# Performance work log

Hardware: AMD Instinct MI355X
Metric: run time of the kernel (lower is better)

Reference implementation:

```python
import jax, jax.numpy as jnp
import numpy as np

DIM = 384
HEADS = 6
NEG = -1e9  # masked-score fill; equivalent to gathering only kept K/V rows


def setup_inputs() -> dict:
    key = jax.random.key(0)
    ks = jax.random.split(key, 9)
    B, N, C = 1, 4098, DIM
    x = jax.random.normal(ks[0], (B, N, C), dtype=jnp.float32)
    pos = jax.random.normal(ks[1], (B, N + 1, C), dtype=jnp.float32)
    # float mask in [0,1); >=0.5 means 'foreground / keep as key', <0.5 pooled into back token
    mask = jax.random.uniform(ks[2], (B, 1, N - 2), dtype=jnp.float32)
    mask_block = jnp.ones((N + 1,), dtype=jnp.float32)  # positions 0, N-1, N always kept
    Wq = jax.random.normal(ks[3], (C, C), dtype=jnp.float32) * 0.02
    Wk = jax.random.normal(ks[4], (C, C), dtype=jnp.float32) * 0.02
    Wv = jax.random.normal(ks[5], (C, C), dtype=jnp.float32) * 0.02
    Wp = jax.random.normal(ks[6], (C, C), dtype=jnp.float32) * 0.02
    bp = jnp.zeros((C,), dtype=jnp.float32)
    return {"x": x, "pos": pos, "mask": mask, "mask_block": mask_block,
            "Wq": Wq, "Wk": Wk, "Wv": Wv, "Wp": Wp, "bp": bp}


def reference(x, pos, mask, mask_block, Wq, Wk, Wv, Wp, bp):
    B, N, C = x.shape
    H = HEADS
    D = C // H
    scale = D ** -0.5
    eps = 1e-10

    # back token: average of background (mask < 0.5) interior tokens
    reverse = jnp.where(mask < 0.5, 1.0, 0.0)                      # (B,1,N-2)
    pooled = jnp.einsum('bon,bnc->boc', reverse, x[:, 1:N - 1])    # (B,1,C)
    back_tokens = pooled / (reverse.sum(axis=2, keepdims=True) + eps)

    kv_x = jnp.concatenate([x, back_tokens], axis=1)               # (B,N+1,C)
    q_x = x + pos[:, :N]
    k_x = kv_x + pos

    q = (q_x @ Wq.T).reshape(B, N, H, D).transpose(0, 2, 1, 3)       # (B,H,N,D)
    k = (k_x @ Wk.T).reshape(B, N + 1, H, D).transpose(0, 2, 1, 3)   # (B,H,N+1,D)
    v = (kv_x @ Wv.T).reshape(B, N + 1, H, D).transpose(0, 2, 1, 3)  # (B,H,N+1,D)

    # key-selection mask: original gathers rows with mask_block >= 0.5;
    # masked softmax over all N+1 keys is mathematically identical.
    mb = mask_block.at[1:N - 1].set(mask[0, 0])
    keep = mb >= 0.5                                               # (N+1,)

    scores = jnp.einsum('bhqd,bhkd->bhqk', q, k) * scale
    scores = jnp.where(keep[None, None, None, :], scores, NEG)
    attn = jax.nn.softmax(scores, axis=-1)
    out = jnp.einsum('bhqk,bhkd->bhqd', attn, v)
    out = out.transpose(0, 2, 1, 3).reshape(B, N, C)
    return out @ Wp.T + bp
```

## Files before the change

kernel.cpp:

```cpp
#include <hip/hip_runtime.h>
#include <math.h>

#define N_TOK 4098
#define NK_TOK 4099
#define C_DIM 384
#define NKPAD 4160
#define NSLICE 5

typedef short  bh8 __attribute__((ext_vector_type(8)));
typedef float  f32x4 __attribute__((ext_vector_type(4)));
typedef unsigned short ushort;
typedef ushort u4 __attribute__((ext_vector_type(4)));
typedef ushort u8 __attribute__((ext_vector_type(8)));

static __device__ __forceinline__ ushort f2bf(float f) {
  unsigned int u = __float_as_uint(f);
  u = (u + 0x7FFF + ((u >> 16) & 1)) >> 16;
  return (ushort)u;
}
static __device__ __forceinline__ float bf2f(ushort s) {
  return __uint_as_float(((unsigned int)s) << 16);
}

#define QSCALE 0.18033688011112042f

__global__ __launch_bounds__(384) void pool_kernel(
    const float* __restrict__ x, const float* __restrict__ mask,
    float* __restrict__ pooled_part, float* __restrict__ cnt_part) {
  const int b = blockIdx.x, t = threadIdx.x;
  const int r0 = b * 32;
  float acc = 0.f;
  int lc = 0;
  for (int r = r0; r < r0 + 32; ++r)
    if (mask[r] < 0.5f) { acc += x[(size_t)(r + 1) * C_DIM + t]; ++lc; }
  pooled_part[b * C_DIM + t] = acc;
  if (t == 0) cnt_part[b] = (float)lc;
}

__global__ __launch_bounds__(256) void prep_kernel(
    const float* __restrict__ x, const float* __restrict__ pos,
    const float* __restrict__ pooled_part, const float* __restrict__ cnt_part,
    const float* __restrict__ Wq, const float* __restrict__ Wk,
    const float* __restrict__ Wv, const float* __restrict__ Wp,
    const float* __restrict__ mask, const float* __restrict__ mask_block,
    ushort* __restrict__ Aq, ushort* __restrict__ Ak, ushort* __restrict__ Av,
    ushort* __restrict__ Wb, int* __restrict__ nk, int* __restrict__ inv) {
  const int b = blockIdx.x, t = threadIdx.x;
  if (b < 260) {
    __shared__ float sback[C_DIM];
    if (b == 256) {
      float cs = 0.f;
      for (int i = (t & 63); i < 128; i += 64) cs += cnt_part[i];
#pragma unroll
      for (int d = 1; d < 64; d <<= 1) cs += __shfl_xor(cs, d);
      const float ic = 1.f / (cs + 1e-10f);
      for (int c = t; c < C_DIM; c += 256) {
        float s = 0.f;
        for (int p = 0; p < 128; ++p) s += pooled_part[p * C_DIM + c];
        sback[c] = s * ic;
      }
      __syncthreads();
    }
    const int r0 = b * 16;
#pragma unroll
    for (int i = 0; i < 6; ++i) {
      const int idx = i * 1024 + t * 4;
      const int row = r0 + idx / C_DIM, col = idx % C_DIM;
      if (row >= NK_TOK) continue;
      const float4 pv = *(const float4*)&pos[(size_t)row * C_DIM + col];
      float4 xv;
      if (row == NK_TOK - 1)
        xv = make_float4(sback[col], sback[col + 1], sback[col + 2], sback[col + 3]);
      else
        xv = *(const float4*)&x[(size_t)row * C_DIM + col];
      if (row < N_TOK) {
        u4 q4 = {f2bf((xv.x + pv.x) * QSCALE), f2bf((xv.y + pv.y) * QSCALE),
                 f2bf((xv.z + pv.z) * QSCALE), f2bf((xv.w + pv.w) * QSCALE)};
        *(u4*)&Aq[(size_t)row * C_DIM + col] = q4;
      }
      u4 k4 = {f2bf(xv.x + pv.x), f2bf(xv.y + pv.y),
               f2bf(xv.z + pv.z), f2bf(xv.w + pv.w)};
      *(u4*)&Ak[(size_t)row * C_DIM + col] = k4;
      u4 v4 = {f2bf(xv.x), f2bf(xv.y), f2bf(xv.z), f2bf(xv.w)};
      *(u4*)&Av[(size_t)row * C_DIM + col] = v4;
    }
  } else if (b < 292) {
    const int wi = b - 260;
    const float* src = (wi < 8) ? Wq : (wi < 16) ? Wk : (wi < 24) ? Wv : Wp;
    const int base = (wi >> 3) * 147456 + (wi & 7) * 18432;
#pragma unroll 2
    for (int i = 0; i < 18; ++i) {
      const int g = base + i * 1024 + t * 4;
      const float4 v = *(const float4*)&src[(wi & 7) * 18432 + i * 1024 + t * 4];
      u4 o = {f2bf(v.x), f2bf(v.y), f2bf(v.z), f2bf(v.w)};
      *(u4*)&Wb[g] = o;
    }
  } else {
    __shared__ int scnt[256];
    const int j0 = t * 17;
    unsigned int bits = 0;
    int c = 0;
#pragma unroll 1
    for (int u = 0; u < 17; ++u) {
      const int j = j0 + u;
      bool keep = false;
      if (j < NK_TOK)
        keep = (j >= 1 && j <= N_TOK - 2) ? (mask[j - 1] >= 0.5f)
                                          : (mask_block[j] >= 0.5f);
      if (keep) { bits |= 1u << u; ++c; }
    }
    scnt[t] = c;
    __syncthreads();
    for (int d = 1; d < 256; d <<= 1) {
      const int v = scnt[t];
      const int add = (t >= d) ? scnt[t - d] : 0;
      __syncthreads();
      scnt[t] = v + add;
      __syncthreads();
    }
    int base = scnt[t] - c;
    if (t == 255) *nk = scnt[255];
#pragma unroll 1
    for (int u = 0; u < 17; ++u) {
      const int j = j0 + u;
      if (j < NK_TOK) inv[j] = ((bits >> u) & 1) ? base++ : -1;
    }
  }
}

static __device__ __forceinline__ void gemm_core(
    const ushort* __restrict__ A, const ushort* __restrict__ B,
    ushort (* __restrict__ As)[72], ushort (* __restrict__ Bs)[72],
    int t, int w, int quad, int l15, f32x4 acc[4]) {
  const int g = t & 7;
  u8 ra[2], rb[2];
#pragma unroll
  for (int it = 0; it < 2; ++it) {
    const int r = it * 32 + (t >> 3);
    ra[it] = *(const u8*)&A[r * C_DIM + g * 8];
    rb[it] = *(const u8*)&B[r * C_DIM + g * 8];
  }
#pragma unroll 1
  for (int kt = 0; kt < 6; ++kt) {
    __syncthreads();
#pragma unroll
    for (int it = 0; it < 2; ++it) {
      const int r = it * 32 + (t >> 3);
      *(u8*)&As[r][g * 8] = ra[it];
      *(u8*)&Bs[r][g * 8] = rb[it];
    }
    __syncthreads();
    if (kt < 5) {
      const int k0 = (kt + 1) * 64;
#pragma unroll
      for (int it = 0; it < 2; ++it) {
        const int r = it * 32 + (t >> 3);
        ra[it] = *(const u8*)&A[r * C_DIM + k0 + g * 8];
        rb[it] = *(const u8*)&B[r * C_DIM + k0 + g * 8];
      }
    }
    const bh8 b0 = *(const bh8*)&Bs[w * 16 + l15][quad * 8];
    const bh8 b1 = *(const bh8*)&Bs[w * 16 + l15][32 + quad * 8];
#pragma unroll
    for (int mb = 0; mb < 4; ++mb) {
      const bh8 a0 = *(const bh8*)&As[mb * 16 + l15][quad * 8];
      const bh8 a1 = *(const bh8*)&As[mb * 16 + l15][32 + quad * 8];
      acc[mb] = __builtin_amdgcn_mfma_f32_16x16x32_bf16(a0, b0, acc[mb], 0, 0, 0);
      acc[mb] = __builtin_amdgcn_mfma_f32_16x16x32_bf16(a1, b1, acc[mb], 0, 0, 0);
    }
  }
}

__global__ __launch_bounds__(256) void gemm3_kernel(
    const ushort* __restrict__ Aq, const ushort* __restrict__ Ak,
    const ushort* __restrict__ Av, const ushort* __restrict__ Wb,
    const int* __restrict__ inv, ushort* __restrict__ Qh,
    ushort* __restrict__ Kc, ushort* __restrict__ Vt) {
  __shared__ ushort As[64][72], Bs[64][72];
  const int t = threadIdx.x, w = t >> 6, lane = t & 63;
  const int quad = lane >> 4, l15 = lane & 15;
  const int m0 = blockIdx.x * 64;
  const int which = blockIdx.y / 6, h = blockIdx.y % 6;
  const ushort* A = (which == 0 ? Aq : which == 1 ? Ak : Av) + (size_t)m0 * C_DIM;
  const ushort* B = Wb + (size_t)which * 147456 + (size_t)h * 64 * C_DIM;
  f32x4 acc[4];
#pragma unroll
  for (int i = 0; i < 4; ++i) acc[i] = (f32x4){0.f, 0.f, 0.f, 0.f};
  gemm_core(A, B, As, Bs, t, w, quad, l15, acc);
  const int n = w * 16 + l15;
  if (which == 0) {
#pragma unroll
    for (int mb = 0; mb < 4; ++mb)
#pragma unroll
      for (int r = 0; r < 4; ++r) {
        const int m = m0 + mb * 16 + quad * 4 + r;
        if (m < N_TOK) Qh[((size_t)h * N_TOK + m) * 64 + n] = f2bf(acc[mb][r]);
      }
  } else if (which == 1) {
#pragma unroll
    for (int mb = 0; mb < 4; ++mb)
#pragma unroll
      for (int r = 0; r < 4; ++r) {
        const int m = m0 + mb * 16 + quad * 4 + r;
        if (m < NK_TOK) {
          const int slot = inv[m];
          if (slot >= 0) Kc[((size_t)h * NKPAD + slot) * 64 + n] = f2bf(acc[mb][r]);
        }
      }
  } else {
#pragma unroll
    for (int mb = 0; mb < 4; ++mb)
#pragma unroll
      for (int r = 0; r < 4; ++r) {
        const int m = m0 + mb * 16 + quad * 4 + r;
        if (m < NK_TOK) {
          const int slot = inv[m];
          if (slot >= 0) Vt[((size_t)h * 64 + n) * NKPAD + slot] = f2bf(acc[mb][r]);
        }
      }
  }
}

__global__ __launch_bounds__(256) void gemm_out_kernel(
    const ushort* __restrict__ Am, const ushort* __restrict__ Wpb,
    const float* __restrict__ bp, float* __restrict__ out) {
  __shared__ ushort As[64][72], Bs[64][72];
  const int t = threadIdx.x, w = t >> 6, lane = t & 63;
  const int quad = lane >> 4, l15 = lane & 15;
  const int m0 = blockIdx.x * 64;
  const int h = blockIdx.y;
  f32x4 acc[4];
#pragma unroll
  for (int i = 0; i < 4; ++i) acc[i] = (f32x4){0.f, 0.f, 0.f, 0.f};
  gemm_core(Am + (size_t)m0 * C_DIM, Wpb + (size_t)h * 64 * C_DIM,
            As, Bs, t, w, quad, l15, acc);
  const int n = w * 16 + l15;
  const float bb = bp[h * 64 + n];
#pragma unroll
  for (int mb = 0; mb < 4; ++mb)
#pragma unroll
    for (int r = 0; r < 4; ++r) {
      const int m = m0 + mb * 16 + quad * 4 + r;
      if (m < N_TOK) out[(size_t)m * C_DIM + h * 64 + n] = acc[mb][r] + bb;
    }
}

__global__ __launch_bounds__(512) void attn_kernel(
    const ushort* __restrict__ Qh, const ushort* __restrict__ Kc,
    const ushort* __restrict__ Vt, const int* __restrict__ nkp,
    ushort* __restrict__ Opart, float* __restrict__ Lpart) {
  __shared__ ushort Ks[64][72];
  __shared__ ushort Vs[64][72];
  __shared__ ushort Ps[8][32][72];
  const int t = threadIdx.x, w = t >> 6, lane = t & 63;
  const int quad = lane >> 4, l15 = lane & 15;
  const int h = blockIdx.y, slice = blockIdx.z;
  const int q0 = blockIdx.x * 256;
  const int nk = *nkp, nchunk = (nk + 63) >> 6;
  const int g = t & 7;
  const int sr = t >> 3;

  bh8 qf[2][2];
#pragma unroll
  for (int qa = 0; qa < 2; ++qa) {
    int qr = q0 + w * 32 + qa * 16 + l15;
    if (qr > N_TOK - 1) qr = N_TOK - 1;
    const ushort* qp = Qh + ((size_t)h * N_TOK + qr) * 64 + quad * 8;
    qf[qa][0] = *(const bh8*)qp;
    qf[qa][1] = *(const bh8*)(qp + 32);
  }
  f32x4 oacc[2][4];
#pragma unroll
  for (int qa = 0; qa < 2; ++qa)
#pragma unroll
    for (int i = 0; i < 4; ++i) oacc[qa][i] = (f32x4){0.f, 0.f, 0.f, 0.f};
  float l_r[2] = {0.f, 0.f};

  const ushort* kb = Kc + (size_t)h * NKPAD * 64;
  const ushort* vb = Vt + (size_t)h * 64 * NKPAD;

  const ushort* kstage = kb + ((size_t)slice * 64 + sr) * 64 + g * 8;
  const ushort* vstage = vb + (size_t)sr * NKPAD + slice * 64 + g * 8;

  u8 rk, rv;
  if (slice < nchunk) {
    rk = *(const u8*)kstage;
    rv = *(const u8*)vstage;
  }
#pragma unroll 1
  for (int kc = slice; kc < nchunk; kc += NSLICE) {
    __syncthreads();
    *(u8*)&Ks[sr][g * 8] = rk;
    *(u8*)&Vs[sr][g * 8] = rv;
    __syncthreads();
    if (kc + NSLICE < nchunk) {
      kstage += NSLICE * 64 * 64;
      vstage += NSLICE * 64;
      rk = *(const u8*)kstage;
      rv = *(const u8*)vstage;
    }
    float csum[2] = {0.f, 0.f};
#pragma unroll
    for (int f = 0; f < 4; ++f) {
      const bh8 a0 = *(const bh8*)&Ks[f * 16 + l15][quad * 8];
      const bh8 a1 = *(const bh8*)&Ks[f * 16 + l15][32 + quad * 8];
      f32x4 s4[2];
#pragma unroll
      for (int qa = 0; qa < 2; ++qa) {
        s4[qa] = (f32x4){0.f, 0.f, 0.f, 0.f};
        s4[qa] = __builtin_amdgcn_mfma_f32_16x16x32_bf16(a0, qf[qa][0], s4[qa], 0, 0, 0);
        s4[qa] = __builtin_amdgcn_mfma_f32_16x16x32_bf16(a1, qf[qa][1], s4[qa], 0, 0, 0);
      }
      const int keyb = kc * 64 + f * 16 + quad * 4;
#pragma unroll
      for (int qa = 0; qa < 2; ++qa) {
        const float p0 = (keyb + 0 < nk) ? __builtin_amdgcn_exp2f(s4[qa][0]) : 0.f;
        const float p1 = (keyb + 1 < nk) ? __builtin_amdgcn_exp2f(s4[qa][1]) : 0.f;
        const float p2 = (keyb + 2 < nk) ? __builtin_amdgcn_exp2f(s4[qa][2]) : 0.f;
        const float p3 = (keyb + 3 < nk) ? __builtin_amdgcn_exp2f(s4[qa][3]) : 0.f;
        csum[qa] += (p0 + p1) + (p2 + p3);
        unsigned int lo, hi;
        asm("v_cvt_pk_bf16_f32 %0, %1, %2" : "=v"(lo) : "v"(p0), "v"(p1));
        asm("v_cvt_pk_bf16_f32 %0, %1, %2" : "=v"(hi) : "v"(p2), "v"(p3));
        uint2 pk;
        pk.x = lo; pk.y = hi;
        *(uint2*)&Ps[w][qa * 16 + l15][f * 16 + quad * 4] = pk;
      }
    }
#pragma unroll
    for (int qa = 0; qa < 2; ++qa) {
      csum[qa] += __shfl_xor(csum[qa], 16);
      csum[qa] += __shfl_xor(csum[qa], 32);
      l_r[qa] += csum[qa];
    }

    bh8 pa[2][2];
#pragma unroll
    for (int qa = 0; qa < 2; ++qa) {
      pa[qa][0] = *(const bh8*)&Ps[w][qa * 16 + l15][quad * 8];
      pa[qa][1] = *(const bh8*)&Ps[w][qa * 16 + l15][32 + quad * 8];
    }
#pragma unroll
    for (int db = 0; db < 4; ++db) {
      const bh8 b0 = *(const bh8*)&Vs[db * 16 + l15][quad * 8];
      const bh8 b1 = *(const bh8*)&Vs[db * 16 + l15][32 + quad * 8];
#pragma unroll
      for (int qa = 0; qa < 2; ++qa) {
        oacc[qa][db] = __builtin_amdgcn_mfma_f32_16x16x32_bf16(pa[qa][0], b0, oacc[qa][db], 0, 0, 0);
        oacc[qa][db] = __builtin_amdgcn_mfma_f32_16x16x32_bf16(pa[qa][1], b1, oacc[qa][db], 0, 0, 0);
      }
    }
  }

  const int sh = slice * 6 + h;
#pragma unroll
  for (int qa = 0; qa < 2; ++qa) {
    const int qg = q0 + w * 32 + qa * 16;
#pragma unroll
    for (int db = 0; db < 4; ++db)
#pragma unroll
      for (int r = 0; r < 4; ++r) {
        const int q = qg + quad * 4 + r;
        if (q < N_TOK)
          Opart[((size_t)sh * NKPAD + q) * 64 + db * 16 + l15] = f2bf(oacc[qa][db][r]);
      }
    if (quad == 0) {
      const int q = qg + l15;
      if (q < N_TOK) Lpart[sh * NKPAD + q] = l_r[qa];
    }
  }
}

__global__ __launch_bounds__(256) void merge_kernel(const ushort* __restrict__ Opart,
                                                    const float* __restrict__ Lpart,
                                                    ushort* __restrict__ Am) {
  const int idx = blockIdx.x * 256 + threadIdx.x;
  if (idx >= N_TOK * 48) return;
  const int q = idx / 48, c = (idx % 48) * 8;
  const int h = c >> 6, d = c & 63;
  float l = 0.f;
#pragma unroll
  for (int s = 0; s < NSLICE; ++s) l += Lpart[(s * 6 + h) * NKPAD + q];
  const float inv = 1.f / l;
  float o[8] = {0.f, 0.f, 0.f, 0.f, 0.f, 0.f, 0.f, 0.f};
#pragma unroll
  for (int s = 0; s < NSLICE; ++s) {
    const u8 v = *(const u8*)&Opart[((size_t)(s * 6 + h) * NKPAD + q) * 64 + d];
#pragma unroll
    for (int j = 0; j < 8; ++j) o[j] += bf2f(v[j]);
  }
  u8 r;
#pragma unroll
  for (int j = 0; j < 8; ++j) r[j] = f2bf(o[j] * inv);
  *(u8*)&Am[(size_t)q * C_DIM + c] = r;
}

extern "C" void kernel_launch(void* const* d_in, const int* in_sizes, int n_in,
                              void* d_out, int out_size, void* d_ws, size_t ws_size,
                              hipStream_t stream) {
  const float* x          = (const float*)d_in[0];
  const float* pos        = (const float*)d_in[1];
  const float* mask       = (const float*)d_in[2];
  const float* mask_block = (const float*)d_in[3];
  const float* Wq         = (const float*)d_in[4];
  const float* Wk         = (const float*)d_in[5];
  const float* Wv         = (const float*)d_in[6];
  const float* Wp         = (const float*)d_in[7];
  const float* bp         = (const float*)d_in[8];
  float* out = (float*)d_out;
  char* wsb = (char*)d_ws;

  float*  pooled_part = (float*)wsb;
  float*  cnt_part    = (float*)(wsb + 196608);
  int*    nk          = (int*)(wsb + 197120);
  int*    inv         = (int*)(wsb + 197632);
  ushort* Aq          = (ushort*)(wsb + 215296);
  ushort* Ak          = (ushort*)(wsb + 3410176);
  ushort* Av          = (ushort*)(wsb + 6605056);
  ushort* Wb          = (ushort*)(wsb + 9799936);
  ushort* Qh          = (ushort*)(wsb + 10979584);
  ushort* Kc          = (ushort*)(wsb + 14126848);
  ushort* Vt          = (ushort*)(wsb + 17321728);
  ushort* Am          = (ushort*)(wsb + 24011008);
  ushort* Op          = (ushort*)(wsb + 27205888);
  float*  Lp          = (float*)(wsb + 46375168);

  pool_kernel<<<dim3(128), dim3(384), 0, stream>>>(x, mask, pooled_part, cnt_part);
  prep_kernel<<<dim3(293), dim3(256), 0, stream>>>(x, pos, pooled_part, cnt_part,
                                                   Wq, Wk, Wv, Wp, mask, mask_block,
                                                   Aq, Ak, Av, Wb, nk, inv);
  gemm3_kernel<<<dim3(65, 18), 256, 0, stream>>>(Aq, Ak, Av, Wb, inv, Qh, Kc, Vt);
  attn_kernel<<<dim3(17, 6, NSLICE), 512, 0, stream>>>(Qh, Kc, Vt, nk, Op, Lp);
  merge_kernel<<<dim3(769), 256, 0, stream>>>(Op, Lp, Am);
  gemm_out_kernel<<<dim3(65, 6), 256, 0, stream>>>(Am, Wb + 3 * 147456, bp, out);
}
```

Baseline: 150.4 us.

## Fold pooling into prep kernel, drop Aq buffer, fold Q scale into Wq

Q input x+pos is identical to K input for the first N rows, so the separate Aq buffer is removed and the query scale is folded into the bf16 Wq conversion, letting the Q GEMM read Ak directly. The pooling pass is merged into prep_kernel as extra blocks, and the back-token row is written afterwards by a tiny single-block kernel. This cuts one bf16 activation write and read and overlaps pooling with the other prep work, at the cost of an extra tiny serial launch.

```diff
diff --git a/kernel.cpp b/kernel.cpp
--- a/kernel.cpp
+++ b/kernel.cpp
@@ -24,60 +24,24 @@
 
 #define QSCALE 0.18033688011112042f
 
-__global__ __launch_bounds__(384) void pool_kernel(
-    const float* __restrict__ x, const float* __restrict__ mask,
-    float* __restrict__ pooled_part, float* __restrict__ cnt_part) {
-  const int b = blockIdx.x, t = threadIdx.x;
-  const int r0 = b * 32;
-  float acc = 0.f;
-  int lc = 0;
-  for (int r = r0; r < r0 + 32; ++r)
-    if (mask[r] < 0.5f) { acc += x[(size_t)(r + 1) * C_DIM + t]; ++lc; }
-  pooled_part[b * C_DIM + t] = acc;
-  if (t == 0) cnt_part[b] = (float)lc;
-}
-
 __global__ __launch_bounds__(256) void prep_kernel(
     const float* __restrict__ x, const float* __restrict__ pos,
-    const float* __restrict__ pooled_part, const float* __restrict__ cnt_part,
     const float* __restrict__ Wq, const float* __restrict__ Wk,
     const float* __restrict__ Wv, const float* __restrict__ Wp,
     const float* __restrict__ mask, const float* __restrict__ mask_block,
-    ushort* __restrict__ Aq, ushort* __restrict__ Ak, ushort* __restrict__ Av,
-    ushort* __restrict__ Wb, int* __restrict__ nk, int* __restrict__ inv) {
+    ushort* __restrict__ Ak, ushort* __restrict__ Av,
+    ushort* __restrict__ Wb, int* __restrict__ nk, int* __restrict__ inv,
+    float* __restrict__ pooled_part, float* __restrict__ cnt_part) {
   const int b = blockIdx.x, t = threadIdx.x;
   if (b < 260) {
-    __shared__ float sback[C_DIM];
-    if (b == 256) {
-      float cs = 0.f;
-      for (int i = (t & 63); i < 128; i += 64) cs += cnt_part[i];
-#pragma unroll
-      for (int d = 1; d < 64; d <<= 1) cs += __shfl_xor(cs, d);
-      const float ic = 1.f / (cs + 1e-10f);
-      for (int c = t; c < C_DIM; c += 256) {
-        float s = 0.f;
-        for (int p = 0; p < 128; ++p) s += pooled_part[p * C_DIM + c];
-        sback[c] = s * ic;
-      }
-      __syncthreads();
-    }
     const int r0 = b * 16;
 #pragma unroll
     for (int i = 0; i < 6; ++i) {
       const int idx = i * 1024 + t * 4;
       const int row = r0 + idx / C_DIM, col = idx % C_DIM;
-      if (row >= NK_TOK) continue;
+      if (row >= NK_TOK - 1) continue;
       const float4 pv = *(const float4*)&pos[(size_t)row * C_DIM + col];
-      float4 xv;
-      if (row == NK_TOK - 1)
-        xv = make_float4(sback[col], sback[col + 1], sback[col + 2], sback[col + 3]);
-      else
-        xv = *(const float4*)&x[(size_t)row * C_DIM + col];
-      if (row < N_TOK) {
-        u4 q4 = {f2bf((xv.x + pv.x) * QSCALE), f2bf((xv.y + pv.y) * QSCALE),
-                 f2bf((xv.z + pv.z) * QSCALE), f2bf((xv.w + pv.w) * QSCALE)};
-        *(u4*)&Aq[(size_t)row * C_DIM + col] = q4;
-      }
+      const float4 xv = *(const float4*)&x[(size_t)row * C_DIM + col];
       u4 k4 = {f2bf(xv.x + pv.x), f2bf(xv.y + pv.y),
                f2bf(xv.z + pv.z), f2bf(xv.w + pv.w)};
       *(u4*)&Ak[(size_t)row * C_DIM + col] = k4;
@@ -87,15 +51,16 @@
   } else if (b < 292) {
     const int wi = b - 260;
     const float* src = (wi < 8) ? Wq : (wi < 16) ? Wk : (wi < 24) ? Wv : Wp;
+    const float sc = (wi < 8) ? QSCALE : 1.f;
     const int base = (wi >> 3) * 147456 + (wi & 7) * 18432;
 #pragma unroll 2
     for (int i = 0; i < 18; ++i) {
       const int g = base + i * 1024 + t * 4;
       const float4 v = *(const float4*)&src[(wi & 7) * 18432 + i * 1024 + t * 4];
-      u4 o = {f2bf(v.x), f2bf(v.y), f2bf(v.z), f2bf(v.w)};
+      u4 o = {f2bf(v.x * sc), f2bf(v.y * sc), f2bf(v.z * sc), f2bf(v.w * sc)};
       *(u4*)&Wb[g] = o;
     }
-  } else {
+  } else if (b == 292) {
     __shared__ int scnt[256];
     const int j0 = t * 17;
     unsigned int bits = 0;
@@ -125,7 +90,39 @@
       const int j = j0 + u;
       if (j < NK_TOK) inv[j] = ((bits >> u) & 1) ? base++ : -1;
     }
-  }
+  } else {
+    const int pb = b - 293;
+    const int r0 = pb * 64;
+    float acc0 = 0.f, acc1 = 0.f;
+    int lc = 0;
+    for (int r = r0; r < r0 + 64; ++r) {
+      if (mask[r] < 0.5f) {
+        acc0 += x[(size_t)(r + 1) * C_DIM + t];
+        if (t < 128) acc1 += x[(size_t)(r + 1) * C_DIM + 256 + t];
+        ++lc;
+      }
+    }
+    pooled_part[pb * C_DIM + t] = acc0;
+    if (t < 128) pooled_part[pb * C_DIM + 256 + t] = acc1;
+    if (t == 0) cnt_part[pb] = (float)lc;
+  }
+}
+
+__global__ __launch_bounds__(384) void back_kernel(
+    const float* __restrict__ pooled_part, const float* __restrict__ cnt_part,
+    const float* __restrict__ pos, ushort* __restrict__ Ak,
+    ushort* __restrict__ Av) {
+  const int t = threadIdx.x;
+  float cs = 0.f;
+#pragma unroll
+  for (int p = 0; p < 64; ++p) cs += cnt_part[p];
+  const float ic = 1.f / (cs + 1e-10f);
+  float s = 0.f;
+  for (int p = 0; p < 64; ++p) s += pooled_part[p * C_DIM + t];
+  const float back = s * ic;
+  const size_t off = (size_t)(NK_TOK - 1) * C_DIM + t;
+  Av[off] = f2bf(back);
+  Ak[off] = f2bf(back + pos[off]);
 }
 
 static __device__ __forceinline__ void gemm_core(
@@ -172,16 +169,15 @@
 }
 
 __global__ __launch_bounds__(256) void gemm3_kernel(
-    const ushort* __restrict__ Aq, const ushort* __restrict__ Ak,
-    const ushort* __restrict__ Av, const ushort* __restrict__ Wb,
-    const int* __restrict__ inv, ushort* __restrict__ Qh,
-    ushort* __restrict__ Kc, ushort* __restrict__ Vt) {
+    const ushort* __restrict__ Ak, const ushort* __restrict__ Av,
+    const ushort* __restrict__ Wb, const int* __restrict__ inv,
+    ushort* __restrict__ Qh, ushort* __restrict__ Kc, ushort* __restrict__ Vt) {
   __shared__ ushort As[64][72], Bs[64][72];
   const int t = threadIdx.x, w = t >> 6, lane = t & 63;
   const int quad = lane >> 4, l15 = lane & 15;
   const int m0 = blockIdx.x * 64;
   const int which = blockIdx.y / 6, h = blockIdx.y % 6;
-  const ushort* A = (which == 0 ? Aq : which == 1 ? Ak : Av) + (size_t)m0 * C_DIM;
+  const ushort* A = (which == 2 ? Av : Ak) + (size_t)m0 * C_DIM;
   const ushort* B = Wb + (size_t)which * 147456 + (size_t)h * 64 * C_DIM;
   f32x4 acc[4];
 #pragma unroll
@@ -411,25 +407,26 @@
   char* wsb = (char*)d_ws;
 
   float*  pooled_part = (float*)wsb;
-  float*  cnt_part    = (float*)(wsb + 196608);
-  int*    nk          = (int*)(wsb + 197120);
-  int*    inv         = (int*)(wsb + 197632);
-  ushort* Aq          = (ushort*)(wsb + 215296);
-  ushort* Ak          = (ushort*)(wsb + 3410176);
-  ushort* Av          = (ushort*)(wsb + 6605056);
-  ushort* Wb          = (ushort*)(wsb + 9799936);
-  ushort* Qh          = (ushort*)(wsb + 10979584);
-  ushort* Kc          = (ushort*)(wsb + 14126848);
-  ushort* Vt          = (ushort*)(wsb + 17321728);
-  ushort* Am          = (ushort*)(wsb + 24011008);
-  ushort* Op          = (ushort*)(wsb + 27205888);
-  float*  Lp          = (float*)(wsb + 46375168);
-
-  pool_kernel<<<dim3(128), dim3(384), 0, stream>>>(x, mask, pooled_part, cnt_part);
-  prep_kernel<<<dim3(293), dim3(256), 0, stream>>>(x, pos, pooled_part, cnt_part,
-                                                   Wq, Wk, Wv, Wp, mask, mask_block,
-                                                   Aq, Ak, Av, Wb, nk, inv);
-  gemm3_kernel<<<dim3(65, 18), 256, 0, stream>>>(Aq, Ak, Av, Wb, inv, Qh, Kc, Vt);
+  float*  cnt_part    = (float*)(wsb + 98304);
+  int*    nk          = (int*)(wsb + 98560);
+  int*    inv         = (int*)(wsb + 99072);
+  ushort* Ak          = (ushort*)(wsb + 115712);
+  ushort* Av          = (ushort*)(wsb + 3310592);
+  ushort* Wb          = (ushort*)(wsb + 6505472);
+  ushort* Qh          = (ushort*)(wsb + 7685120);
+  ushort* Kc          = (ushort*)(wsb + 10832384);
+  ushort* Vt          = (ushort*)(wsb + 14027264);
+  ushort* Am          = (ushort*)(wsb + 17222144);
+  ushort* Op          = (ushort*)(wsb + 20417024);
+  float*  Lp          = (float*)(wsb + 36391424);
+
+  prep_kernel<<<dim3(357), dim3(256), 0, stream>>>(x, pos, Wq, Wk, Wv, Wp,
+                                                   mask, mask_block, Ak, Av,
+                                                   Wb, nk, inv,
+                                                   pooled_part, cnt_part);
+  back_kernel<<<dim3(1), dim3(384), 0, stream>>>(pooled_part, cnt_part, pos,
+                                                 Ak, Av);
+  gemm3_kernel<<<dim3(65, 18), 256, 0, stream>>>(Ak, Av, Wb, inv, Qh, Kc, Vt);
   attn_kernel<<<dim3(17, 6, NSLICE), 512, 0, stream>>>(Qh, Kc, Vt, nk, Op, Lp);
   merge_kernel<<<dim3(769), 256, 0, stream>>>(Op, Lp, Am);
   gemm_out_kernel<<<dim3(65, 6), 256, 0, stream>>>(Am, Wb + 3 * 147456, bp, out);
```

After: 148.1 us. Within noise of the previous version (-1.6%).
